# Kernel tuning notes

Measured on AMD Instinct MI355X. Metric: run time of the kernel, lower is better.

The kernel has to match this reference:

```python
import jax, jax.numpy as jnp
import numpy as np

UNITS = 512

def setup_inputs() -> dict:
    key = jax.random.key(0)
    ks = jax.random.split(key, 7)
    B, T, D, U = 64, 2048, 256, UNITS
    return {
        "x":   jax.random.normal(ks[0], (B, T, D), dtype=jnp.float32),
        "Wk":  jax.random.normal(ks[1], (D, 2 * U), dtype=jnp.float32) * 0.05,
        "Wrk": jax.random.normal(ks[2], (U, 2 * U), dtype=jnp.float32) * 0.05,
        "brk": jnp.zeros((2 * U,), dtype=jnp.float32),
        "Wu":  jax.random.normal(ks[3], (D, U), dtype=jnp.float32) * 0.05,
        "Wur": jax.random.normal(ks[4], (U, U), dtype=jnp.float32) * 0.05,
        "bur": jnp.zeros((U,), dtype=jnp.float32),
    }

def reference(x, Wk, Wrk, brk, Wu, Wur, bur):
    B, T, D = x.shape
    U = Wu.shape[1]
    # Precompute all input projections in two batched GEMMs (fuse over time).
    xz = jnp.einsum('btd,dk->btk', x, Wk)   # [B, T, 2U]
    xu = jnp.einsum('btd,du->btu', x, Wu)   # [B, T, U]
    h0 = jnp.zeros((B, U), dtype=x.dtype)

    def step(h, inp):
        xz_t, xu_t = inp                      # [B,2U], [B,U]
        z = xz_t + h @ Wrk + brk              # [B, 2U]
        r_t = jax.nn.sigmoid(z[:, :U])
        z_t = jax.nn.sigmoid(z[:, U:])
        h_t = jnp.tanh(xu_t + (h * r_t) @ Wur + bur)
        h_new = (1.0 - z_t) * h + z_t * h_t
        return h_new, None

    # scan over time axis
    xz_t = jnp.swapaxes(xz, 0, 1)  # [T, B, 2U]
    xu_t = jnp.swapaxes(xu, 0, 1)  # [T, B, U]
    h_final, _ = jax.lax.scan(step, h0, (xz_t, xu_t))
    return h_final  # [B, U] — original returns stacked states sliced to last step
```

## Files before the change

kernel.cpp:

```cpp
#include <hip/hip_runtime.h>


#define TT 2048
#define DD 256
#define UU 512

typedef short bf16x8 __attribute__((ext_vector_type(8)));
typedef float f32x4 __attribute__((ext_vector_type(4)));
typedef unsigned int u32;
typedef unsigned long long u64;

#define H_OFF 0
#define HR_OFF 131072
#define FLAG_OFF 262144
#define WS_BYTES 266240

__device__ inline unsigned short f2bf(float f) {
  unsigned u = __builtin_bit_cast(unsigned, f);
  u += 0x7FFFu + ((u >> 16) & 1u);
  return (unsigned short)(u >> 16);
}
__device__ inline float bf2f(unsigned short b) {
  unsigned u = ((unsigned)b) << 16;
  return __builtin_bit_cast(float, u);
}
__device__ inline u32 ld_coh_u32(const u32* p) {
  return __hip_atomic_load(p, __ATOMIC_RELAXED, __HIP_MEMORY_SCOPE_AGENT);
}
__device__ inline u64 ld_coh_u64(const u64* p) {
  return __hip_atomic_load(p, __ATOMIC_RELAXED, __HIP_MEMORY_SCOPE_AGENT);
}
__device__ inline void st_coh_u32(u32* p, u32 v) {
  __hip_atomic_store(p, v, __ATOMIC_RELAXED, __HIP_MEMORY_SCOPE_AGENT);
}

#define MFMA(A, B, C) __builtin_amdgcn_mfma_f32_16x16x32_bf16((A), (B), (C), 0, 0, 0)

__global__ __launch_bounds__(256, 1) void gru_persist(
    const float* __restrict__ x, const float* __restrict__ Wk,
    const float* __restrict__ Wrk, const float* __restrict__ brk,
    const float* __restrict__ Wu, const float* __restrict__ Wur,
    const float* __restrict__ bur, float* __restrict__ out,
    unsigned char* __restrict__ ws) {
  __shared__ float scratch[24576];

  const int wg = blockIdx.x;
  const int bblk = wg & 3;
  const int cb = wg >> 2;
  const bool zwg = (cb >= 32);
  const int tid = threadIdx.x;
  const int lane = tid & 63;
  const int wv = tid >> 6;
  const int kgrp = lane >> 4;
  const int c = lane & 15;

  const int P1C0 = cb * 16;
  const int P2C0 = zwg ? (cb - 32) * 16 : 0;

  u32* h_pack = (u32*)(ws + H_OFF);
  u32* hr_pack = (u32*)(ws + HR_OFF);
  u32* flags = (u32*)(ws + FLAG_OFF) + bblk * 256;

  bf16x8 w1hi[6], w1lo[6], w2hi[6], w2lo[6];
#pragma unroll
  for (int j = 0; j < 6; ++j) {
    const int kb = (wv + 4 * j) * 32 + kgrp * 8;
#pragma unroll
    for (int i = 0; i < 8; ++i) {
      const int k = kb + i;
      float v = (k < DD) ? Wk[(size_t)k * 1024 + P1C0 + c]
                         : Wrk[(size_t)(k - DD) * 1024 + P1C0 + c];
      unsigned short hb = f2bf(v);
      w1hi[j][i] = (short)hb;
      w1lo[j][i] = (short)f2bf(v - bf2f(hb));
      float v2 = 0.f;
      if (zwg)
        v2 = (k < DD) ? Wu[(size_t)k * UU + P2C0 + c]
                      : Wur[(size_t)(k - DD) * UU + P2C0 + c];
      unsigned short hb2 = f2bf(v2);
      w2hi[j][i] = (short)hb2;
      w2lo[j][i] = (short)f2bf(v2 - bf2f(hb2));
    }
  }

  const int bl = tid >> 4, cl = tid & 15;
  const int Bg = bblk * 16 + bl;
  const float b1 = brk[P1C0 + cl];
  const float b2 = zwg ? bur[P2C0 + cl] : 0.f;

  const int rowb = bblk * 16 + c;

  bf16x8 xhi[2], xlo[2];
  auto split_x = [&](int t) {
#pragma unroll
    for (int j = 0; j < 2; ++j) {
      const float* xr =
          x + ((size_t)rowb * TT + t) * DD + wv * 32 + j * 128 + kgrp * 8;
      f32x4 v0 = *(const f32x4*)(xr);
      f32x4 v1 = *(const f32x4*)(xr + 4);
#pragma unroll
      for (int i = 0; i < 4; ++i) {
        unsigned short hb = f2bf(v0[i]);
        xhi[j][i] = (short)hb;
        xlo[j][i] = (short)f2bf(v0[i] - bf2f(hb));
        unsigned short hb2 = f2bf(v1[i]);
        xhi[j][4 + i] = (short)hb2;
        xlo[j][4 + i] = (short)f2bf(v1[i] - bf2f(hb2));
      }
    }
  };
  split_x(0);

  auto gemm = [&](const u32* pack, const bf16x8* whi,
                  const bf16x8* wlo) -> f32x4 {
    u64 q[4][4];
#pragma unroll
    for (int j = 0; j < 4; ++j) {
      const int k0 = wv * 32 + j * 128 + kgrp * 8;
      const u64* src = (const u64*)(pack + (size_t)rowb * UU + k0);
      q[j][0] = ld_coh_u64(src + 0);
      q[j][1] = ld_coh_u64(src + 1);
      q[j][2] = ld_coh_u64(src + 2);
      q[j][3] = ld_coh_u64(src + 3);
    }
    f32x4 a0 = {0.f, 0.f, 0.f, 0.f}, a1 = {0.f, 0.f, 0.f, 0.f};
    a0 = MFMA(xhi[0], whi[0], a0);
    a0 = MFMA(xhi[0], wlo[0], a0);
    a0 = MFMA(xlo[0], whi[0], a0);
    a1 = MFMA(xhi[1], whi[1], a1);
    a1 = MFMA(xhi[1], wlo[1], a1);
    a1 = MFMA(xlo[1], whi[1], a1);
#pragma unroll
    for (int j = 0; j < 4; ++j) {
      bf16x8 ahi, alo;
#pragma unroll
      for (int i = 0; i < 4; ++i) {
        u32 lo32 = (u32)q[j][i];
        u32 hi32 = (u32)(q[j][i] >> 32);
        ahi[2 * i] = (short)(lo32 >> 16);
        alo[2 * i] = (short)lo32;
        ahi[2 * i + 1] = (short)(hi32 >> 16);
        alo[2 * i + 1] = (short)hi32;
      }
      if ((j & 1) == 0) {
        a0 = MFMA(ahi, whi[j + 2], a0);
        a0 = MFMA(ahi, wlo[j + 2], a0);
        a0 = MFMA(alo, whi[j + 2], a0);
      } else {
        a1 = MFMA(ahi, whi[j + 2], a1);
        a1 = MFMA(ahi, wlo[j + 2], a1);
        a1 = MFMA(alo, whi[j + 2], a1);
      }
    }
    return a0 + a1;
  };

  unsigned bar = 0;
  for (int t = 0; t < TT; ++t) {
    u32 hp = 0;
    if (!zwg) hp = ld_coh_u32(h_pack + (size_t)Bg * UU + P1C0 + cl);
    f32x4 acc = gemm(h_pack, w1hi, w1lo);
#pragma unroll
    for (int r = 0; r < 4; ++r)
      scratch[wv * 256 + (kgrp * 4 + r) * 16 + c] = acc[r];
    __syncthreads();
    {
      float z = (scratch[tid] + scratch[256 + tid]) +
                (scratch[512 + tid] + scratch[768 + tid]) + b1;
      float s = 1.f / (1.f + __expf(-z));
      if (!zwg) {
        float h = bf2f((unsigned short)(hp >> 16)) + bf2f((unsigned short)hp);
        float hrv = h * s;
        unsigned short hb = f2bf(hrv);
        unsigned short lb = f2bf(hrv - bf2f(hb));
        st_coh_u32(hr_pack + (size_t)Bg * UU + P1C0 + cl,
                   ((u32)hb << 16) | lb);
      }
      float zt = s;

      asm volatile("s_waitcnt vmcnt(0)" ::: "memory");
      __syncthreads();
      ++bar;
      if (tid == 0) st_coh_u32(flags + cb * 4, bar);
      if (wv == 0) {
        const u32* fp = flags + lane * 4;
        while (!__all(ld_coh_u32(fp) >= bar)) {
        }
      }
      __syncthreads();

      if (zwg) {
        u32 hp2 = ld_coh_u32(h_pack + (size_t)Bg * UU + P2C0 + cl);
        f32x4 acc2 = gemm(hr_pack, w2hi, w2lo);
#pragma unroll
        for (int r = 0; r < 4; ++r)
          scratch[wv * 256 + (kgrp * 4 + r) * 16 + c] = acc2[r];
        __syncthreads();
        float u = (scratch[tid] + scratch[256 + tid]) +
                  (scratch[512 + tid] + scratch[768 + tid]) + b2;
        float e = __expf(2.f * u);
        float ht = 1.f - 2.f / (e + 1.f);
        float ho = bf2f((unsigned short)(hp2 >> 16)) + bf2f((unsigned short)hp2);
        float hn = ho + zt * (ht - ho);
        unsigned short hb = f2bf(hn);
        unsigned short lb = f2bf(hn - bf2f(hb));
        st_coh_u32(h_pack + (size_t)Bg * UU + P2C0 + cl, ((u32)hb << 16) | lb);
        if (t == TT - 1) out[(size_t)Bg * UU + P2C0 + cl] = hn;
      }

      asm volatile("s_waitcnt vmcnt(0)" ::: "memory");
      __syncthreads();
      ++bar;
      if (tid == 0) st_coh_u32(flags + cb * 4, bar);
      if (t + 1 < TT) split_x(t + 1);
      if (wv == 0) {
        const u32* fp = flags + lane * 4;
        while (!__all(ld_coh_u32(fp) >= bar)) {
        }
      }
      __syncthreads();
    }
  }
}

extern "C" void kernel_launch(void* const* d_in, const int* in_sizes, int n_in,
                              void* d_out, int out_size, void* d_ws,
                              size_t ws_size, hipStream_t stream) {
  (void)in_sizes; (void)n_in; (void)out_size; (void)ws_size;
  hipMemsetAsync(d_ws, 0, WS_BYTES, stream);
  gru_persist<<<dim3(256), dim3(256), 0, stream>>>(
      (const float*)d_in[0], (const float*)d_in[1], (const float*)d_in[2],
      (const float*)d_in[3], (const float*)d_in[4], (const float*)d_in[5],
      (const float*)d_in[6], (float*)d_out, (unsigned char*)d_ws);
}
```

Before: 16.41 ms.

## Restructure persistent GRU into 64 blocks with per-wave flag sync and double-buffered state

Shrinks the grid from 256 to 64 workgroups, each wave independently handling a 16-row batch slice across the full K=768 reduction, which removes the LDS cross-wave reduction and block-level __syncthreads. The kernel now has separate r-role and z-role blocks that synchronise through per-wave flags, with h and h*r double-buffered by timestep parity so the z-role blocks can overlap with the next step. Low-half weights move to LDS, and z-role blocks keep the previous h in registers instead of reloading it. In exchange each wave does a longer serial chain of MFMAs and global loads per step, and fewer CUs are used.

```diff
diff --git a/kernel.cpp b/kernel.cpp
--- a/kernel.cpp
+++ b/kernel.cpp
@@ -10,10 +10,11 @@
 typedef unsigned int u32;
 typedef unsigned long long u64;
 
-#define H_OFF 0
-#define HR_OFF 131072
-#define FLAG_OFF 262144
-#define WS_BYTES 266240
+#define H2_OFF 0
+#define HR2_OFF 262144
+#define ZF_OFF 524288
+#define RF_OFF 532480
+#define WS_BYTES 540672
 
 __device__ inline unsigned short f2bf(float f) {
   unsigned u = __builtin_bit_cast(unsigned, f);
@@ -42,62 +43,67 @@
     const float* __restrict__ Wu, const float* __restrict__ Wur,
     const float* __restrict__ bur, float* __restrict__ out,
     unsigned char* __restrict__ ws) {
-  __shared__ float scratch[24576];
-
-  const int wg = blockIdx.x;
-  const int bblk = wg & 3;
-  const int cb = wg >> 2;
-  const bool zwg = (cb >= 32);
+  __shared__ short wsh[49152];
+
+  const int b = blockIdx.x;
+  const bool zrole = (b >= 32);
   const int tid = threadIdx.x;
   const int lane = tid & 63;
-  const int wv = tid >> 6;
+  const int g = tid >> 6;
   const int kgrp = lane >> 4;
   const int c = lane & 15;
 
-  const int P1C0 = cb * 16;
-  const int P2C0 = zwg ? (cb - 32) * 16 : 0;
-
-  u32* h_pack = (u32*)(ws + H_OFF);
-  u32* hr_pack = (u32*)(ws + HR_OFF);
-  u32* flags = (u32*)(ws + FLAG_OFF) + bblk * 256;
-
-  bf16x8 w1hi[6], w1lo[6], w2hi[6], w2lo[6];
-#pragma unroll
-  for (int j = 0; j < 6; ++j) {
-    const int kb = (wv + 4 * j) * 32 + kgrp * 8;
-#pragma unroll
-    for (int i = 0; i < 8; ++i) {
-      const int k = kb + i;
-      float v = (k < DD) ? Wk[(size_t)k * 1024 + P1C0 + c]
-                         : Wrk[(size_t)(k - DD) * 1024 + P1C0 + c];
-      unsigned short hb = f2bf(v);
-      w1hi[j][i] = (short)hb;
-      w1lo[j][i] = (short)f2bf(v - bf2f(hb));
-      float v2 = 0.f;
-      if (zwg)
-        v2 = (k < DD) ? Wu[(size_t)k * UU + P2C0 + c]
-                      : Wur[(size_t)(k - DD) * UU + P2C0 + c];
+  const int C1 = zrole ? 512 + (b - 32) * 16 : b * 16;
+  const int C2 = zrole ? (b - 32) * 16 : 0;
+
+  for (int idx = tid; idx < 12288; idx += 256) {
+    int k = idx >> 4, cc = idx & 15;
+    int ad = (k >> 5) * 512 + ((k >> 3) & 3) * 128 + cc * 8 + (k & 7);
+    float v = (k < DD) ? Wk[(size_t)k * 1024 + C1 + cc]
+                       : Wrk[(size_t)(k - DD) * 1024 + C1 + cc];
+    unsigned short hb = f2bf(v);
+    wsh[ad] = (short)hb;
+    wsh[12288 + ad] = (short)f2bf(v - bf2f(hb));
+    if (zrole) {
+      float v2 = (k < DD) ? Wu[(size_t)k * UU + C2 + cc]
+                          : Wur[(size_t)(k - DD) * UU + C2 + cc];
       unsigned short hb2 = f2bf(v2);
-      w2hi[j][i] = (short)hb2;
-      w2lo[j][i] = (short)f2bf(v2 - bf2f(hb2));
+      wsh[24576 + ad] = (short)hb2;
+      wsh[36864 + ad] = (short)f2bf(v2 - bf2f(hb2));
     }
   }
-
-  const int bl = tid >> 4, cl = tid & 15;
-  const int Bg = bblk * 16 + bl;
-  const float b1 = brk[P1C0 + cl];
-  const float b2 = zwg ? bur[P2C0 + cl] : 0.f;
-
-  const int rowb = bblk * 16 + c;
-
-  bf16x8 xhi[2], xlo[2];
+  __syncthreads();
+
+  bf16x8 w1hi[24];
+#pragma unroll
+  for (int j = 0; j < 24; ++j)
+    w1hi[j] = *(const bf16x8*)&wsh[j * 512 + lane * 8];
+  bf16x8 w2hi[24];
+  if (zrole) {
+#pragma unroll
+    for (int j = 0; j < 24; ++j)
+      w2hi[j] = *(const bf16x8*)&wsh[24576 + j * 512 + lane * 8];
+  }
+
+  u32* h2p = (u32*)(ws + H2_OFF);
+  u32* hr2p = (u32*)(ws + HR2_OFF);
+  u32* zfg = (u32*)(ws + ZF_OFF) + g * 512;
+  u32* rfg = (u32*)(ws + RF_OFF) + g * 512;
+  const int ti = zrole ? b - 32 : b;
+  u32* myflag = (zrole ? zfg : rfg) + ti * 16;
+
+  const float b1 = brk[C1 + c];
+  const float b2 = zrole ? bur[C2 + c] : 0.f;
+
+  const float* xrow = x + (size_t)(16 * g + c) * TT * DD;
+
+  bf16x8 xhi[8], xlo[8];
   auto split_x = [&](int t) {
 #pragma unroll
-    for (int j = 0; j < 2; ++j) {
-      const float* xr =
-          x + ((size_t)rowb * TT + t) * DD + wv * 32 + j * 128 + kgrp * 8;
-      f32x4 v0 = *(const f32x4*)(xr);
-      f32x4 v1 = *(const f32x4*)(xr + 4);
+    for (int j = 0; j < 8; ++j) {
+      const float* p = xrow + (size_t)t * DD + j * 32 + kgrp * 8;
+      f32x4 v0 = *(const f32x4*)p;
+      f32x4 v1 = *(const f32x4*)(p + 4);
 #pragma unroll
       for (int i = 0; i < 4; ++i) {
         unsigned short hb = f2bf(v0[i]);
@@ -109,116 +115,118 @@
       }
     }
   };
-  split_x(0);
-
-  auto gemm = [&](const u32* pack, const bf16x8* whi,
-                  const bf16x8* wlo) -> f32x4 {
-    u64 q[4][4];
-#pragma unroll
-    for (int j = 0; j < 4; ++j) {
-      const int k0 = wv * 32 + j * 128 + kgrp * 8;
-      const u64* src = (const u64*)(pack + (size_t)rowb * UU + k0);
-      q[j][0] = ld_coh_u64(src + 0);
-      q[j][1] = ld_coh_u64(src + 1);
-      q[j][2] = ld_coh_u64(src + 2);
-      q[j][3] = ld_coh_u64(src + 3);
-    }
-    f32x4 a0 = {0.f, 0.f, 0.f, 0.f}, a1 = {0.f, 0.f, 0.f, 0.f};
-    a0 = MFMA(xhi[0], whi[0], a0);
-    a0 = MFMA(xhi[0], wlo[0], a0);
-    a0 = MFMA(xlo[0], whi[0], a0);
-    a1 = MFMA(xhi[1], whi[1], a1);
-    a1 = MFMA(xhi[1], wlo[1], a1);
-    a1 = MFMA(xlo[1], whi[1], a1);
-#pragma unroll
-    for (int j = 0; j < 4; ++j) {
+
+  auto waitflags = [&](const u32* f, u32 need) {
+    const u32* p = f + (lane & 31) * 16;
+    while (!__all(ld_coh_u32(p) >= need)) __builtin_amdgcn_s_sleep(1);
+  };
+
+  auto gemm768 = [&](const u32* rowbase, const bf16x8* whi,
+                     int loreg) -> f32x4 {
+    f32x4 ac0 = {0.f, 0.f, 0.f, 0.f}, ac1 = ac0, ac2 = ac0, ac3 = ac0;
+#pragma unroll
+    for (int j = 0; j < 8; ++j) {
+      bf16x8 blo = *(const bf16x8*)&wsh[loreg + j * 512 + lane * 8];
+      f32x4& a = (j & 3) == 0 ? ac0 : ((j & 3) == 1 ? ac1 : ((j & 3) == 2 ? ac2 : ac3));
+      a = MFMA(xhi[j], whi[j], a);
+      a = MFMA(xhi[j], blo, a);
+      a = MFMA(xlo[j], whi[j], a);
+    }
+    u64 Q[4][4];
+#pragma unroll
+    for (int p = 0; p < 4; ++p) {
+      const u64* s = (const u64*)(rowbase + p * 32 + kgrp * 8);
+      Q[p][0] = ld_coh_u64(s + 0); Q[p][1] = ld_coh_u64(s + 1);
+      Q[p][2] = ld_coh_u64(s + 2); Q[p][3] = ld_coh_u64(s + 3);
+    }
+#pragma unroll
+    for (int j = 0; j < 16; ++j) {
       bf16x8 ahi, alo;
 #pragma unroll
       for (int i = 0; i < 4; ++i) {
-        u32 lo32 = (u32)q[j][i];
-        u32 hi32 = (u32)(q[j][i] >> 32);
+        u32 lo32 = (u32)Q[j & 3][i], hi32 = (u32)(Q[j & 3][i] >> 32);
         ahi[2 * i] = (short)(lo32 >> 16);
         alo[2 * i] = (short)lo32;
         ahi[2 * i + 1] = (short)(hi32 >> 16);
         alo[2 * i + 1] = (short)hi32;
       }
-      if ((j & 1) == 0) {
-        a0 = MFMA(ahi, whi[j + 2], a0);
-        a0 = MFMA(ahi, wlo[j + 2], a0);
-        a0 = MFMA(alo, whi[j + 2], a0);
-      } else {
-        a1 = MFMA(ahi, whi[j + 2], a1);
-        a1 = MFMA(ahi, wlo[j + 2], a1);
-        a1 = MFMA(alo, whi[j + 2], a1);
-      }
-    }
-    return a0 + a1;
+      if (j + 4 < 16) {
+        const u64* s = (const u64*)(rowbase + (j + 4) * 32 + kgrp * 8);
+        Q[j & 3][0] = ld_coh_u64(s + 0); Q[j & 3][1] = ld_coh_u64(s + 1);
+        Q[j & 3][2] = ld_coh_u64(s + 2); Q[j & 3][3] = ld_coh_u64(s + 3);
+      }
+      bf16x8 blo = *(const bf16x8*)&wsh[loreg + (8 + j) * 512 + lane * 8];
+      f32x4& a = (j & 3) == 0 ? ac0 : ((j & 3) == 1 ? ac1 : ((j & 3) == 2 ? ac2 : ac3));
+      a = MFMA(ahi, whi[8 + j], a);
+      a = MFMA(ahi, blo, a);
+      a = MFMA(alo, whi[8 + j], a);
+    }
+    return (ac0 + ac1) + (ac2 + ac3);
   };
 
-  unsigned bar = 0;
+  split_x(0);
+  float hnprev[4] = {0.f, 0.f, 0.f, 0.f};
+
   for (int t = 0; t < TT; ++t) {
-    u32 hp = 0;
-    if (!zwg) hp = ld_coh_u32(h_pack + (size_t)Bg * UU + P1C0 + cl);
-    f32x4 acc = gemm(h_pack, w1hi, w1lo);
-#pragma unroll
-    for (int r = 0; r < 4; ++r)
-      scratch[wv * 256 + (kgrp * 4 + r) * 16 + c] = acc[r];
-    __syncthreads();
-    {
-      float z = (scratch[tid] + scratch[256 + tid]) +
-                (scratch[512 + tid] + scratch[768 + tid]) + b1;
-      float s = 1.f / (1.f + __expf(-z));
-      if (!zwg) {
-        float h = bf2f((unsigned short)(hp >> 16)) + bf2f((unsigned short)hp);
-        float hrv = h * s;
+    const int bh = (t + 1) & 1;
+
+    waitflags(zfg, (u32)t);
+    u32 oh0 = 0, oh1 = 0, oh2 = 0, oh3 = 0;
+    if (!zrole) {
+      const u32* q =
+          h2p + ((size_t)(bh * 64 + 16 * g + 4 * (lane >> 4))) * 512 + C1 + c;
+      oh0 = ld_coh_u32(q);       oh1 = ld_coh_u32(q + 512);
+      oh2 = ld_coh_u32(q + 1024); oh3 = ld_coh_u32(q + 1536);
+    }
+    const u32* hrow = h2p + ((size_t)(bh * 64 + 16 * g + c)) * 512;
+    f32x4 acc = gemm768(hrow, w1hi, 12288);
+    float s0 = 1.f / (1.f + __expf(-(acc[0] + b1)));
+    float s1 = 1.f / (1.f + __expf(-(acc[1] + b1)));
+    float s2 = 1.f / (1.f + __expf(-(acc[2] + b1)));
+    float s3 = 1.f / (1.f + __expf(-(acc[3] + b1)));
+
+    if (!zrole) {
+      u32* dst =
+          hr2p + ((size_t)((t & 1) * 64 + 16 * g + 4 * (lane >> 4))) * 512 +
+          C1 + c;
+      u32 ohs[4] = {oh0, oh1, oh2, oh3};
+      float ss[4] = {s0, s1, s2, s3};
+#pragma unroll
+      for (int ri = 0; ri < 4; ++ri) {
+        float h = bf2f((unsigned short)(ohs[ri] >> 16)) +
+                  bf2f((unsigned short)ohs[ri]);
+        float hrv = h * ss[ri];
         unsigned short hb = f2bf(hrv);
         unsigned short lb = f2bf(hrv - bf2f(hb));
-        st_coh_u32(hr_pack + (size_t)Bg * UU + P1C0 + cl,
-                   ((u32)hb << 16) | lb);
-      }
-      float zt = s;
-
+        st_coh_u32(dst + ri * 512, ((u32)hb << 16) | lb);
+      }
       asm volatile("s_waitcnt vmcnt(0)" ::: "memory");
-      __syncthreads();
-      ++bar;
-      if (tid == 0) st_coh_u32(flags + cb * 4, bar);
-      if (wv == 0) {
-        const u32* fp = flags + lane * 4;
-        while (!__all(ld_coh_u32(fp) >= bar)) {
-        }
-      }
-      __syncthreads();
-
-      if (zwg) {
-        u32 hp2 = ld_coh_u32(h_pack + (size_t)Bg * UU + P2C0 + cl);
-        f32x4 acc2 = gemm(hr_pack, w2hi, w2lo);
-#pragma unroll
-        for (int r = 0; r < 4; ++r)
-          scratch[wv * 256 + (kgrp * 4 + r) * 16 + c] = acc2[r];
-        __syncthreads();
-        float u = (scratch[tid] + scratch[256 + tid]) +
-                  (scratch[512 + tid] + scratch[768 + tid]) + b2;
-        float e = __expf(2.f * u);
+      if (lane == 0) st_coh_u32(myflag, (u32)(t + 1));
+      if (t + 1 < TT) split_x(t + 1);
+    } else {
+      waitflags(rfg, (u32)(t + 1));
+      const u32* hrrow = hr2p + ((size_t)((t & 1) * 64 + 16 * g + c)) * 512;
+      f32x4 uacc = gemm768(hrrow, w2hi, 36864);
+      u32* dst =
+          h2p + ((size_t)((t & 1) * 64 + 16 * g + 4 * (lane >> 4))) * 512 +
+          C2 + c;
+      float zz[4] = {s0, s1, s2, s3};
+#pragma unroll
+      for (int ri = 0; ri < 4; ++ri) {
+        float uv = uacc[ri] + b2;
+        float e = __expf(2.f * uv);
         float ht = 1.f - 2.f / (e + 1.f);
-        float ho = bf2f((unsigned short)(hp2 >> 16)) + bf2f((unsigned short)hp2);
-        float hn = ho + zt * (ht - ho);
+        float hn = hnprev[ri] + zz[ri] * (ht - hnprev[ri]);
+        hnprev[ri] = hn;
         unsigned short hb = f2bf(hn);
         unsigned short lb = f2bf(hn - bf2f(hb));
-        st_coh_u32(h_pack + (size_t)Bg * UU + P2C0 + cl, ((u32)hb << 16) | lb);
-        if (t == TT - 1) out[(size_t)Bg * UU + P2C0 + cl] = hn;
-      }
-
+        st_coh_u32(dst + ri * 512, ((u32)hb << 16) | lb);
+        if (t == TT - 1)
+          out[(size_t)(16 * g + 4 * (lane >> 4) + ri) * UU + C2 + c] = hn;
+      }
       asm volatile("s_waitcnt vmcnt(0)" ::: "memory");
-      __syncthreads();
-      ++bar;
-      if (tid == 0) st_coh_u32(flags + cb * 4, bar);
+      if (lane == 0) st_coh_u32(myflag, (u32)(t + 1));
       if (t + 1 < TT) split_x(t + 1);
-      if (wv == 0) {
-        const u32* fp = flags + lane * 4;
-        while (!__all(ld_coh_u32(fp) >= bar)) {
-        }
-      }
-      __syncthreads();
     }
   }
 }
@@ -228,7 +236,7 @@
                               size_t ws_size, hipStream_t stream) {
   (void)in_sizes; (void)n_in; (void)out_size; (void)ws_size;
   hipMemsetAsync(d_ws, 0, WS_BYTES, stream);
-  gru_persist<<<dim3(256), dim3(256), 0, stream>>>(
+  gru_persist<<<dim3(64), dim3(256), 0, stream>>>(
       (const float*)d_in[0], (const float*)d_in[1], (const float*)d_in[2],
       (const float*)d_in[3], (const float*)d_in[4], (const float*)d_in[5],
       (const float*)d_in[6], (float*)d_out, (unsigned char*)d_ws);
```

Result: slower. 35.92 ms (+118.9%).
